# Kernel tuning notes

Measured on AMD Instinct MI355X. Metric: run time of the kernel, lower is better.

The kernel has to match this reference:

```python
import jax, jax.numpy as jnp
import numpy as np

N_VIEWS = 8


def _trilinear(vol, pts):
    """Trilinear interpolation of vol [Nx,Ny,Nz] at pts [...,3] (voxel coords), zero outside."""
    nx, ny, nz = vol.shape
    x, y, z = pts[..., 0], pts[..., 1], pts[..., 2]
    x0f, y0f, z0f = jnp.floor(x), jnp.floor(y), jnp.floor(z)
    fx, fy, fz = x - x0f, y - y0f, z - z0f
    x0 = x0f.astype(jnp.int32)
    y0 = y0f.astype(jnp.int32)
    z0 = z0f.astype(jnp.int32)
    out = jnp.zeros(x.shape, vol.dtype)
    for dx in (0, 1):
        wx = fx if dx else (1.0 - fx)
        ix = x0 + dx
        vx = (ix >= 0) & (ix < nx)
        ixc = jnp.clip(ix, 0, nx - 1)
        for dy in (0, 1):
            wy = fy if dy else (1.0 - fy)
            iy = y0 + dy
            vxy = vx & (iy >= 0) & (iy < ny)
            iyc = jnp.clip(iy, 0, ny - 1)
            for dz in (0, 1):
                wz = fz if dz else (1.0 - fz)
                iz = z0 + dz
                valid = vxy & (iz >= 0) & (iz < nz)
                izc = jnp.clip(iz, 0, nz - 1)
                v = vol[ixc, iyc, izc]  # irregular gather
                out = out + jnp.where(valid, v, jnp.zeros((), vol.dtype)) * (wx * wy * wz)
    return out


def cone_project(vol, src_pos, det_center, det_u_vec, det_v_vec,
                 det_u, det_v, du, dv, voxel_spacing, n_steps):
    """Cone-beam forward projection: ray-march src->detector pixel, trilinear sampling."""
    nx, ny, nz = vol.shape
    us = (jnp.arange(det_u, dtype=vol.dtype) - (det_u - 1) / 2.0) * du
    vs = (jnp.arange(det_v, dtype=vol.dtype) - (det_v - 1) / 2.0) * dv
    # detector pixel world positions: [V, U, W, 3]
    det_pts = (det_center[:, None, None, :]
               + us[None, :, None, None] * det_u_vec[:, None, None, :]
               + vs[None, None, :, None] * det_v_vec[:, None, None, :])
    src = src_pos[:, None, None, :]            # [V,1,1,3]
    diff = det_pts - src                        # [V,U,W,3]
    ray_len = jnp.sqrt(jnp.sum(diff * diff, axis=-1))  # [V,U,W]
    step_len = ray_len / n_steps
    center = (jnp.array([nx, ny, nz], dtype=vol.dtype) - 1.0) / 2.0
    fracs = (jnp.arange(n_steps, dtype=vol.dtype) + 0.5) / n_steps

    def body(acc, s):
        p = src + s * diff                      # world coords [V,U,W,3]
        vox = p / voxel_spacing + center        # voxel coords
        return acc + _trilinear(vol, vox), None

    acc, _ = jax.lax.scan(body, jnp.zeros(ray_len.shape, vol.dtype), fracs)
    return acc * step_len


def setup_inputs() -> dict:
    key = jax.random.key(0)
    k1, k2 = jax.random.split(key)
    vol_shape = (256, 256, 256)
    x = 0.1 * jax.random.normal(k1, vol_shape, dtype=jnp.float32)
    reco = 0.1 * jax.random.normal(k2, vol_shape, dtype=jnp.float32)
    # circular cone-beam trajectory (units = voxels, spacing 1.0)
    sad, sdd = 400.0, 800.0  # source-axis / source-detector distance
    angles = np.linspace(0.0, np.pi, N_VIEWS, endpoint=False)
    ca, sa = np.cos(angles), np.sin(angles)
    zeros = np.zeros(N_VIEWS)
    src_pos = np.stack([-sad * ca, -sad * sa, zeros], axis=-1)
    det_center = np.stack([(sdd - sad) * ca, (sdd - sad) * sa, zeros], axis=-1)
    det_u_vec = np.stack([-sa, ca, zeros], axis=-1)
    det_v_vec = np.tile(np.array([0.0, 0.0, 1.0]), (N_VIEWS, 1))
    return {
        "x": x,
        "reco": reco,
        "src_pos": jnp.asarray(src_pos, jnp.float32),
        "det_center": jnp.asarray(det_center, jnp.float32),
        "det_u_vec": jnp.asarray(det_u_vec, jnp.float32),
        "det_v_vec": jnp.asarray(det_v_vec, jnp.float32),
        "du": 3.0,
        "dv": 3.0,
        "voxel_spacing": 1.0,
        "det_u": 128,
        "det_v": 128,
        "n_steps": 192,
    }


def reference(x, reco, src_pos, det_center, det_u_vec, det_v_vec,
              du, dv, voxel_spacing, det_u, det_v, n_steps):
    updated = x + reco
    sino = cone_project(updated, src_pos, det_center, det_u_vec, det_v_vec,
                        det_u, det_v, du, dv, voxel_spacing, n_steps)
    return sino, jax.nn.relu(updated)
```

## Files before the change

kernel.cpp:

```cpp
#include <hip/hip_runtime.h>
#include <math.h>

__global__ __launch_bounds__(256) void add_relu_kernel(
    const float* __restrict__ x,
    const float* __restrict__ reco,
    float* __restrict__ relu_out,
    float* __restrict__ upd_out,
    int n4)
{
    int i = blockIdx.x * blockDim.x + threadIdx.x;
    int stride = gridDim.x * blockDim.x;
    const float4* x4 = (const float4*)x;
    const float4* r4 = (const float4*)reco;
    float4* ro4 = (float4*)relu_out;
    float4* uo4 = (float4*)upd_out;
    for (; i < n4; i += stride) {
        float4 a = x4[i];
        float4 b = r4[i];
        float4 u;
        u.x = a.x + b.x;
        u.y = a.y + b.y;
        u.z = a.z + b.z;
        u.w = a.w + b.w;
        if (uo4) uo4[i] = u;
        float4 r;
        r.x = fmaxf(u.x, 0.0f);
        r.y = fmaxf(u.y, 0.0f);
        r.z = fmaxf(u.z, 0.0f);
        r.w = fmaxf(u.w, 0.0f);
        ro4[i] = r;
    }
}

template <int TWO>
__device__ __forceinline__ float fetch_corner(
    const float* __restrict__ vol_a,
    const float* __restrict__ vol_b,
    int ix, int iy, int iz,
    int nx, int ny, int nz)
{
    bool valid = (ix >= 0) & (ix < nx) & (iy >= 0) & (iy < ny) &
                 (iz >= 0) & (iz < nz);
    if (!valid) return 0.0f;
    int idx = (ix * ny + iy) * nz + iz;
    float v = vol_a[idx];
    if (TWO) v += vol_b[idx];
    return v;
}

__device__ __forceinline__ void clip_axis(float a, float b, float lo, float hi,
                                          float& t_lo, float& t_hi)
{
    if (fabsf(b) > 1e-6f) {
        float t0 = (lo - a) / b;
        float t1 = (hi - a) / b;
        float tmn = fminf(t0, t1);
        float tmx = fmaxf(t0, t1);
        t_lo = fmaxf(t_lo, tmn);
        t_hi = fminf(t_hi, tmx);
    } else {
        if (a <= lo || a >= hi) { t_lo = 1.0f; t_hi = 0.0f; }
    }
}

template <int TWO>
__global__ __launch_bounds__(256) void cone_project_seg_kernel(
    const float* __restrict__ vol_a,
    const float* __restrict__ vol_b,
    const float* __restrict__ src_pos,
    const float* __restrict__ det_center,
    const float* __restrict__ det_u_vec,
    const float* __restrict__ det_v_vec,
    const float* __restrict__ du_p,
    const float* __restrict__ dv_p,
    const float* __restrict__ spacing_p,
    const int* __restrict__ det_u_p,
    const int* __restrict__ det_v_p,
    const int* __restrict__ nsteps_p,
    float* __restrict__ sino,
    int n_views, int nx, int ny, int nz)
{
    const int det_u = *det_u_p;
    const int det_v = *det_v_p;
    const int n_steps = *nsteps_p;
    const float du = *du_p;
    const float dv = *dv_p;
    const float inv_sp = 1.0f / *spacing_p;

    const long total = (long)n_views * det_u * det_v;
    const int pix = threadIdx.x & 63;
    const int seg = threadIdx.x >> 6;
    const long idx = (long)blockIdx.x * 64 + pix;
    const bool live = idx < total;

    const long cidx = live ? idx : 0;
    const int v = (int)(cidx % det_v);
    const int u = (int)((cidx / det_v) % det_u);
    const int view = (int)(cidx / ((long)det_u * det_v));

    const float us = ((float)u - (det_u - 1) * 0.5f) * du;
    const float vs = ((float)v - (det_v - 1) * 0.5f) * dv;

    const float sx = src_pos[view * 3 + 0];
    const float sy = src_pos[view * 3 + 1];
    const float sz = src_pos[view * 3 + 2];

    const float dpx = det_center[view * 3 + 0] + us * det_u_vec[view * 3 + 0] + vs * det_v_vec[view * 3 + 0];
    const float dpy = det_center[view * 3 + 1] + us * det_u_vec[view * 3 + 1] + vs * det_v_vec[view * 3 + 1];
    const float dpz = det_center[view * 3 + 2] + us * det_u_vec[view * 3 + 2] + vs * det_v_vec[view * 3 + 2];

    const float dx = dpx - sx;
    const float dy = dpy - sy;
    const float dz = dpz - sz;
    const float ray_len = sqrtf(dx * dx + dy * dy + dz * dz);
    const float step_len = ray_len / (float)n_steps;

    const float cx = (nx - 1) * 0.5f;
    const float cy = (ny - 1) * 0.5f;
    const float cz = (nz - 1) * 0.5f;

    float t_lo = 0.0f, t_hi = 1.0f;
    clip_axis(sx * inv_sp + cx, dx * inv_sp, -1.0f, (float)nx, t_lo, t_hi);
    clip_axis(sy * inv_sp + cy, dy * inv_sp, -1.0f, (float)ny, t_lo, t_hi);
    clip_axis(sz * inv_sp + cz, dz * inv_sp, -1.0f, (float)nz, t_lo, t_hi);

    int i_min = 0, i_max = -1;
    if (t_hi > t_lo) {
        i_min = (int)floorf(t_lo * (float)n_steps - 0.5f) - 1;
        i_max = (int)ceilf(t_hi * (float)n_steps - 0.5f) + 1;
        i_min = max(i_min, 0);
        i_max = min(i_max, n_steps - 1);
    }
    if (!live) { i_min = 0; i_max = -1; }

    const int count = i_max - i_min + 1;
    const int per = (count + 3) >> 2;
    const int is = i_min + seg * per;
    const int ie = min(is + per - 1, i_max);

    const float inv_n = 1.0f / (float)n_steps;

    float acc = 0.0f;
    for (int i = is; i <= ie; ++i) {
        const float s = ((float)i + 0.5f) * inv_n;
        const float px = fmaf(s, dx, sx) * inv_sp + cx;
        const float py = fmaf(s, dy, sy) * inv_sp + cy;
        const float pz = fmaf(s, dz, sz) * inv_sp + cz;

        const float x0f = floorf(px);
        const float y0f = floorf(py);
        const float z0f = floorf(pz);
        const float fx = px - x0f;
        const float fy = py - y0f;
        const float fz = pz - z0f;
        const int x0 = (int)x0f;
        const int y0 = (int)y0f;
        const int z0 = (int)z0f;

        const float gx = 1.0f - fx;
        const float gy = 1.0f - fy;
        const float gz = 1.0f - fz;

        float samp = 0.0f;
        samp = fmaf(gx * gy * gz, fetch_corner<TWO>(vol_a, vol_b, x0,     y0,     z0,     nx, ny, nz), samp);
        samp = fmaf(gx * gy * fz, fetch_corner<TWO>(vol_a, vol_b, x0,     y0,     z0 + 1, nx, ny, nz), samp);
        samp = fmaf(gx * fy * gz, fetch_corner<TWO>(vol_a, vol_b, x0,     y0 + 1, z0,     nx, ny, nz), samp);
        samp = fmaf(gx * fy * fz, fetch_corner<TWO>(vol_a, vol_b, x0,     y0 + 1, z0 + 1, nx, ny, nz), samp);
        samp = fmaf(fx * gy * gz, fetch_corner<TWO>(vol_a, vol_b, x0 + 1, y0,     z0,     nx, ny, nz), samp);
        samp = fmaf(fx * gy * fz, fetch_corner<TWO>(vol_a, vol_b, x0 + 1, y0,     z0 + 1, nx, ny, nz), samp);
        samp = fmaf(fx * fy * gz, fetch_corner<TWO>(vol_a, vol_b, x0 + 1, y0 + 1, z0,     nx, ny, nz), samp);
        samp = fmaf(fx * fy * fz, fetch_corner<TWO>(vol_a, vol_b, x0 + 1, y0 + 1, z0 + 1, nx, ny, nz), samp);
        acc += samp;
    }

    __shared__ float red[256];
    red[threadIdx.x] = acc;
    __syncthreads();
    if (seg == 0 && live) {
        float tot = red[pix] + red[pix + 64] + red[pix + 128] + red[pix + 192];
        sino[idx] = tot * step_len;
    }
}

extern "C" void kernel_launch(void* const* d_in, const int* in_sizes, int n_in,
                              void* d_out, int out_size, void* d_ws, size_t ws_size,
                              hipStream_t stream) {
    const float* x          = (const float*)d_in[0];
    const float* reco       = (const float*)d_in[1];
    const float* src_pos    = (const float*)d_in[2];
    const float* det_center = (const float*)d_in[3];
    const float* det_u_vec  = (const float*)d_in[4];
    const float* det_v_vec  = (const float*)d_in[5];
    const float* du_p       = (const float*)d_in[6];
    const float* dv_p       = (const float*)d_in[7];
    const float* spacing_p  = (const float*)d_in[8];
    const int*   det_u_p    = (const int*)d_in[9];
    const int*   det_v_p    = (const int*)d_in[10];
    const int*   nsteps_p   = (const int*)d_in[11];

    const int n_vol = in_sizes[0];
    const int n_views = in_sizes[2] / 3;

    int n = 1;
    while ((long)(n + 1) * (n + 1) * (n + 1) <= (long)n_vol) ++n;
    const int nx = n, ny = n, nz = n;

    const int sino_size = out_size - n_vol;
    float* sino     = (float*)d_out;
    float* relu_out = (float*)d_out + sino_size;

    const bool use_ws = ws_size >= (size_t)n_vol * sizeof(float);
    float* upd = (float*)d_ws;

    const int n4 = n_vol / 4;
    add_relu_kernel<<<2048, 256, 0, stream>>>(
        x, reco, relu_out, use_ws ? upd : nullptr, n4);

    const int blocks = (sino_size + 63) / 64;
    if (use_ws) {
        cone_project_seg_kernel<0><<<blocks, 256, 0, stream>>>(
            upd, nullptr,
            src_pos, det_center, det_u_vec, det_v_vec,
            du_p, dv_p, spacing_p, det_u_p, det_v_p, nsteps_p,
            sino, n_views, nx, ny, nz);
    } else {
        cone_project_seg_kernel<1><<<blocks, 256, 0, stream>>>(
            x, reco,
            src_pos, det_center, det_u_vec, det_v_vec,
            du_p, dv_p, spacing_p, det_u_p, det_v_p, nsteps_p,
            sino, n_views, nx, ny, nz);
    }
}
```

Measured before the change: 238.1 us.

## Split rays into eight segments, add interior fast path, unroll elementwise kernel

The cone projector now assigns 32 rays per block with 8 step segments per ray instead of 64 rays with 4 segments. This raises parallelism per ray and shortens each thread's serial march. The trilinear sampling gets a branch for interior voxels that computes one base address and skips the per-corner bounds checks. Separately, the add+relu kernel loads four float4 pairs up front to raise memory-level parallelism, and its grid is sized to the data. In exchange, each block covers fewer rays, which may reduce gather locality across adjacent pixels, and the reduction is longer.

```diff
diff --git a/kernel.cpp b/kernel.cpp
--- a/kernel.cpp
+++ b/kernel.cpp
@@ -1,5 +1,7 @@
 #include <hip/hip_runtime.h>
 #include <math.h>
+
+typedef float nfloat4 __attribute__((ext_vector_type(4)));
 
 __global__ __launch_bounds__(256) void add_relu_kernel(
     const float* __restrict__ x,
@@ -8,26 +10,47 @@
     float* __restrict__ upd_out,
     int n4)
 {
-    int i = blockIdx.x * blockDim.x + threadIdx.x;
-    int stride = gridDim.x * blockDim.x;
-    const float4* x4 = (const float4*)x;
-    const float4* r4 = (const float4*)reco;
-    float4* ro4 = (float4*)relu_out;
-    float4* uo4 = (float4*)upd_out;
-    for (; i < n4; i += stride) {
-        float4 a = x4[i];
-        float4 b = r4[i];
-        float4 u;
-        u.x = a.x + b.x;
-        u.y = a.y + b.y;
-        u.z = a.z + b.z;
-        u.w = a.w + b.w;
+    const int tid = blockIdx.x * 256 + threadIdx.x;
+    const int S = gridDim.x * 256;
+    const nfloat4* x4 = (const nfloat4*)x;
+    const nfloat4* r4 = (const nfloat4*)reco;
+    nfloat4* ro4 = (nfloat4*)relu_out;
+    nfloat4* uo4 = (nfloat4*)upd_out;
+
+    const int i0 = tid, i1 = tid + S, i2 = tid + 2 * S, i3 = tid + 3 * S;
+
+    const nfloat4 zero = {0.f, 0.f, 0.f, 0.f};
+    nfloat4 a0 = (i0 < n4) ? x4[i0] : zero;
+    nfloat4 b0 = (i0 < n4) ? r4[i0] : zero;
+    nfloat4 a1 = (i1 < n4) ? x4[i1] : zero;
+    nfloat4 b1 = (i1 < n4) ? r4[i1] : zero;
+    nfloat4 a2 = (i2 < n4) ? x4[i2] : zero;
+    nfloat4 b2 = (i2 < n4) ? r4[i2] : zero;
+    nfloat4 a3 = (i3 < n4) ? x4[i3] : zero;
+    nfloat4 b3 = (i3 < n4) ? r4[i3] : zero;
+
+#define DO_ONE(ii, aa, bb)                                                    \
+    if (ii < n4) {                                                            \
+        nfloat4 u = aa + bb;                                                  \
+        if (uo4) uo4[ii] = u;                                                 \
+        nfloat4 r;                                                            \
+        r.x = fmaxf(u.x, 0.f); r.y = fmaxf(u.y, 0.f);                         \
+        r.z = fmaxf(u.z, 0.f); r.w = fmaxf(u.w, 0.f);                         \
+        ro4[ii] = r;                                                          \
+    }
+    DO_ONE(i0, a0, b0)
+    DO_ONE(i1, a1, b1)
+    DO_ONE(i2, a2, b2)
+    DO_ONE(i3, a3, b3)
+#undef DO_ONE
+
+    for (int i = tid + 4 * S; i < n4; i += S) {
+        nfloat4 a = x4[i], b = r4[i];
+        nfloat4 u = a + b;
         if (uo4) uo4[i] = u;
-        float4 r;
-        r.x = fmaxf(u.x, 0.0f);
-        r.y = fmaxf(u.y, 0.0f);
-        r.z = fmaxf(u.z, 0.0f);
-        r.w = fmaxf(u.w, 0.0f);
+        nfloat4 r;
+        r.x = fmaxf(u.x, 0.f); r.y = fmaxf(u.y, 0.f);
+        r.z = fmaxf(u.z, 0.f); r.w = fmaxf(u.w, 0.f);
         ro4[i] = r;
     }
 }
@@ -88,9 +111,9 @@
     const float inv_sp = 1.0f / *spacing_p;
 
     const long total = (long)n_views * det_u * det_v;
-    const int pix = threadIdx.x & 63;
-    const int seg = threadIdx.x >> 6;
-    const long idx = (long)blockIdx.x * 64 + pix;
+    const int pix = threadIdx.x & 31;
+    const int seg = threadIdx.x >> 5;
+    const long idx = (long)blockIdx.x * 32 + pix;
     const bool live = idx < total;
 
     const long cidx = live ? idx : 0;
@@ -134,7 +157,7 @@
     if (!live) { i_min = 0; i_max = -1; }
 
     const int count = i_max - i_min + 1;
-    const int per = (count + 3) >> 2;
+    const int per = (count + 7) >> 3;
     const int is = i_min + seg * per;
     const int ie = min(is + per - 1, i_max);
 
@@ -161,15 +184,51 @@
         const float gy = 1.0f - fy;
         const float gz = 1.0f - fz;
 
+        const bool interior = (x0 >= 0) & (x0 + 1 < nx) &
+                              (y0 >= 0) & (y0 + 1 < ny) &
+                              (z0 >= 0) & (z0 + 1 < nz);
+
         float samp = 0.0f;
-        samp = fmaf(gx * gy * gz, fetch_corner<TWO>(vol_a, vol_b, x0,     y0,     z0,     nx, ny, nz), samp);
-        samp = fmaf(gx * gy * fz, fetch_corner<TWO>(vol_a, vol_b, x0,     y0,     z0 + 1, nx, ny, nz), samp);
-        samp = fmaf(gx * fy * gz, fetch_corner<TWO>(vol_a, vol_b, x0,     y0 + 1, z0,     nx, ny, nz), samp);
-        samp = fmaf(gx * fy * fz, fetch_corner<TWO>(vol_a, vol_b, x0,     y0 + 1, z0 + 1, nx, ny, nz), samp);
-        samp = fmaf(fx * gy * gz, fetch_corner<TWO>(vol_a, vol_b, x0 + 1, y0,     z0,     nx, ny, nz), samp);
-        samp = fmaf(fx * gy * fz, fetch_corner<TWO>(vol_a, vol_b, x0 + 1, y0,     z0 + 1, nx, ny, nz), samp);
-        samp = fmaf(fx * fy * gz, fetch_corner<TWO>(vol_a, vol_b, x0 + 1, y0 + 1, z0,     nx, ny, nz), samp);
-        samp = fmaf(fx * fy * fz, fetch_corner<TWO>(vol_a, vol_b, x0 + 1, y0 + 1, z0 + 1, nx, ny, nz), samp);
+        if (interior) {
+            const int base = (x0 * ny + y0) * nz + z0;
+            const float* pa = vol_a + base;
+            float v000 = pa[0];
+            float v001 = pa[1];
+            float v010 = pa[nz];
+            float v011 = pa[nz + 1];
+            float v100 = pa[ny * nz];
+            float v101 = pa[ny * nz + 1];
+            float v110 = pa[ny * nz + nz];
+            float v111 = pa[ny * nz + nz + 1];
+            if (TWO) {
+                const float* pb = vol_b + base;
+                v000 += pb[0];
+                v001 += pb[1];
+                v010 += pb[nz];
+                v011 += pb[nz + 1];
+                v100 += pb[ny * nz];
+                v101 += pb[ny * nz + 1];
+                v110 += pb[ny * nz + nz];
+                v111 += pb[ny * nz + nz + 1];
+            }
+            samp = fmaf(gx * gy * gz, v000, samp);
+            samp = fmaf(gx * gy * fz, v001, samp);
+            samp = fmaf(gx * fy * gz, v010, samp);
+            samp = fmaf(gx * fy * fz, v011, samp);
+            samp = fmaf(fx * gy * gz, v100, samp);
+            samp = fmaf(fx * gy * fz, v101, samp);
+            samp = fmaf(fx * fy * gz, v110, samp);
+            samp = fmaf(fx * fy * fz, v111, samp);
+        } else {
+            samp = fmaf(gx * gy * gz, fetch_corner<TWO>(vol_a, vol_b, x0,     y0,     z0,     nx, ny, nz), samp);
+            samp = fmaf(gx * gy * fz, fetch_corner<TWO>(vol_a, vol_b, x0,     y0,     z0 + 1, nx, ny, nz), samp);
+            samp = fmaf(gx * fy * gz, fetch_corner<TWO>(vol_a, vol_b, x0,     y0 + 1, z0,     nx, ny, nz), samp);
+            samp = fmaf(gx * fy * fz, fetch_corner<TWO>(vol_a, vol_b, x0,     y0 + 1, z0 + 1, nx, ny, nz), samp);
+            samp = fmaf(fx * gy * gz, fetch_corner<TWO>(vol_a, vol_b, x0 + 1, y0,     z0,     nx, ny, nz), samp);
+            samp = fmaf(fx * gy * fz, fetch_corner<TWO>(vol_a, vol_b, x0 + 1, y0,     z0 + 1, nx, ny, nz), samp);
+            samp = fmaf(fx * fy * gz, fetch_corner<TWO>(vol_a, vol_b, x0 + 1, y0 + 1, z0,     nx, ny, nz), samp);
+            samp = fmaf(fx * fy * fz, fetch_corner<TWO>(vol_a, vol_b, x0 + 1, y0 + 1, z0 + 1, nx, ny, nz), samp);
+        }
         acc += samp;
     }
 
@@ -177,7 +236,8 @@
     red[threadIdx.x] = acc;
     __syncthreads();
     if (seg == 0 && live) {
-        float tot = red[pix] + red[pix + 64] + red[pix + 128] + red[pix + 192];
+        float tot = red[pix]       + red[pix + 32]  + red[pix + 64]  + red[pix + 96] +
+                    red[pix + 128] + red[pix + 160] + red[pix + 192] + red[pix + 224];
         sino[idx] = tot * step_len;
     }
 }
@@ -213,10 +273,11 @@
     float* upd = (float*)d_ws;
 
     const int n4 = n_vol / 4;
-    add_relu_kernel<<<2048, 256, 0, stream>>>(
+    const int ew_blocks = (n4 / 4 + 255) / 256;
+    add_relu_kernel<<<ew_blocks, 256, 0, stream>>>(
         x, reco, relu_out, use_ws ? upd : nullptr, n4);
 
-    const int blocks = (sino_size + 63) / 64;
+    const int blocks = (sino_size + 31) / 32;
     if (use_ws) {
         cone_project_seg_kernel<0><<<blocks, 256, 0, stream>>>(
             upd, nullptr,
```

After: 239.0 us. Within noise of the previous version (+0.4%).
